# Kernel tuning notes

Measured on AMD Instinct MI355X. Metric: run time of the kernel, lower is better.

The kernel has to match this reference:

```python
import jax, jax.numpy as jnp
import numpy as np

B, S, E = 4, 2048, 1024
H, D = 16, 64
SCALE = D ** -0.5


def setup_inputs() -> dict:
    key = jax.random.key(0)
    ks = jax.random.split(key, 6)
    x = jax.random.normal(ks[0], (B, S, E), dtype=jnp.float32)
    # per-head projection weights stacked along head axis: [H, E, D]
    Wq = jax.random.normal(ks[1], (H, E, D), dtype=jnp.float32) * 0.02
    Wk = jax.random.normal(ks[2], (H, E, D), dtype=jnp.float32) * 0.02
    Wv = jax.random.normal(ks[3], (H, E, D), dtype=jnp.float32) * 0.02
    # output projection: concat(H*D) -> E, with bias (nn.Linear default)
    Wo = jax.random.normal(ks[4], (H * D, E), dtype=jnp.float32) * 0.02
    bo = jax.random.normal(ks[5], (E,), dtype=jnp.float32) * 0.02
    return {"x": x, "Wq": Wq, "Wk": Wk, "Wv": Wv, "Wo": Wo, "bo": bo}


def reference(x, Wq, Wk, Wv, Wo, bo):
    # batched QKV projections for all heads at once
    q = jnp.einsum('bse,hed->bhsd', x, Wq)
    k = jnp.einsum('bse,hed->bhsd', x, Wk)
    v = jnp.einsum('bse,hed->bhsd', x, Wv)
    # full (non-causal) attention, scores [b,h,s,s]
    scores = jnp.einsum('bhsd,bhtd->bhst', q, k) * SCALE
    attn = jax.nn.softmax(scores, axis=-1)
    o = jnp.einsum('bhst,bhtd->bhsd', attn, v)
    # concat heads in head order along feature dim -> [b,s,H*D]
    o = o.transpose(0, 2, 1, 3).reshape(x.shape[0], x.shape[1], -1)
    return o @ Wo + bo
```

## Files before the change

### kernel.cpp

```cpp
#include <hip/hip_runtime.h>
#include <hip/hip_fp16.h>
#include <stdint.h>

#define BB 4
#define SS 2048
#define EE 1024
#define HH 16
#define DD 64

typedef _Float16 half8 __attribute__((ext_vector_type(8)));
typedef __fp16 fp16x2 __attribute__((ext_vector_type(2)));
typedef float f32x2 __attribute__((ext_vector_type(2)));
typedef float f32x4 __attribute__((ext_vector_type(4)));
typedef float f32x16 __attribute__((ext_vector_type(16)));
typedef uint32_t u32;
typedef uint32_t u32x2 __attribute__((ext_vector_type(2)));

#define MFMA32(a, b, c) __builtin_amdgcn_mfma_f32_16x16x32_f16((a), (b), (c), 0, 0, 0)
#define MFMA3216(a, b, c) __builtin_amdgcn_mfma_f32_32x32x16_f16((a), (b), (c), 0, 0, 0)

#define GLD_LDS16(g, l)                                                        \
  __builtin_amdgcn_global_load_lds(                                            \
      (const __attribute__((address_space(1))) u32*)(const void*)(g),          \
      (__attribute__((address_space(3))) u32*)(void*)(l), 16, 0, 0)

static __device__ __forceinline__ u32 pkh(float a, float b) {
  union { fp16x2 h; u32 u; } z;
  z.h = __builtin_amdgcn_cvt_pkrtz(a, b);
  return z.u;
}

static __device__ __forceinline__ void plswap(u32& a, u32& b) {
  asm("v_permlane32_swap_b32 %0, %1" : "+v"(a), "+v"(b));
}

__global__ __launch_bounds__(256) void conv_x_k(const float* __restrict__ x,
                                                _Float16* __restrict__ xh) {
  size_t i = ((size_t)blockIdx.x * 256 + threadIdx.x) * 8;
  f32x4 a = *(const f32x4*)(x + i);
  f32x4 b = *(const f32x4*)(x + i + 4);
  half8 o;
  o[0] = (_Float16)a[0]; o[1] = (_Float16)a[1];
  o[2] = (_Float16)a[2]; o[3] = (_Float16)a[3];
  o[4] = (_Float16)b[0]; o[5] = (_Float16)b[1];
  o[6] = (_Float16)b[2]; o[7] = (_Float16)b[3];
  *(half8*)(xh + i) = o;
}

__global__ __launch_bounds__(256) void conv_w_k(const float* __restrict__ Wq,
                                                const float* __restrict__ Wk,
                                                const float* __restrict__ Wv,
                                                _Float16* __restrict__ Wt) {
  __shared__ float T[64][65];
  int bid = blockIdx.x;
  int sel = bid >> 8, rem = bid & 255;
  int h = rem >> 4, e0 = (rem & 15) * 64;
  const float* W = (sel == 0 ? Wq : sel == 1 ? Wk : Wv) + (size_t)h * EE * DD;
  float scale = (sel == 0) ? 0.18033688011112042f : 1.0f;
  int tid = threadIdx.x;
  {
    int e = tid >> 2, d0 = (tid & 3) * 16;
#pragma unroll
    for (int i = 0; i < 4; ++i) {
      f32x4 v = *(const f32x4*)(W + (size_t)(e0 + e) * DD + d0 + i * 4);
      T[e][d0 + i * 4 + 0] = v[0];
      T[e][d0 + i * 4 + 1] = v[1];
      T[e][d0 + i * 4 + 2] = v[2];
      T[e][d0 + i * 4 + 3] = v[3];
    }
  }
  __syncthreads();
  {
    int d = tid >> 2, c0 = (tid & 3) * 16;
    half8 o0, o1;
#pragma unroll
    for (int i = 0; i < 8; ++i) o0[i] = (_Float16)(T[c0 + i][d] * scale);
#pragma unroll
    for (int i = 0; i < 8; ++i) o1[i] = (_Float16)(T[c0 + 8 + i][d] * scale);
    _Float16* dst = Wt + ((size_t)sel * 1024 + h * 64 + d) * EE + e0 + c0;
    *(half8*)dst = o0;
    *(half8*)(dst + 8) = o1;
  }
}

__global__ __launch_bounds__(256) void conv_wo_k(const float* __restrict__ Wo,
                                                 _Float16* __restrict__ Wot) {
  __shared__ float T[64][65];
  int bid = blockIdx.x;
  int k0 = (bid >> 4) * 64, n0 = (bid & 15) * 64;
  int tid = threadIdx.x;
  {
    int k = tid >> 2, c0 = (tid & 3) * 16;
#pragma unroll
    for (int i = 0; i < 4; ++i) {
      f32x4 v = *(const f32x4*)(Wo + (size_t)(k0 + k) * EE + n0 + c0 + i * 4);
      T[k][c0 + i * 4 + 0] = v[0];
      T[k][c0 + i * 4 + 1] = v[1];
      T[k][c0 + i * 4 + 2] = v[2];
      T[k][c0 + i * 4 + 3] = v[3];
    }
  }
  __syncthreads();
  {
    int n = tid >> 2, c0 = (tid & 3) * 16;
    half8 o0, o1;
#pragma unroll
    for (int i = 0; i < 8; ++i) o0[i] = (_Float16)T[c0 + i][n];
#pragma unroll
    for (int i = 0; i < 8; ++i) o1[i] = (_Float16)T[c0 + 8 + i][n];
    _Float16* dst = Wot + (size_t)(n0 + n) * EE + k0 + c0;
    *(half8*)dst = o0;
    *(half8*)(dst + 8) = o1;
  }
}

__global__ __launch_bounds__(256, 3) void qkv_proj_k(
    const _Float16* __restrict__ xh, const _Float16* __restrict__ Wt,
    _Float16* __restrict__ qkv) {
  __shared__ __align__(16) _Float16 As[2][128 * 32];
  __shared__ __align__(16) _Float16 Bs[2][128 * 32];
  __shared__ __align__(16) _Float16 Tt[64][136];
  int bid0 = blockIdx.x;
  int bid = (bid0 & 7) * 192 + (bid0 >> 3);
  int nblk = bid % 24, mblk = bid / 24;
  int row0 = mblk * 128, n0 = nblk * 128;
  int tid = threadIdx.x, lane = tid & 63, w = tid >> 6;
  int wm = w >> 1, wn = w & 1;
  int l15 = lane & 15, lhi = lane >> 4;

  f32x4 acc[4][4];
#pragma unroll
  for (int i = 0; i < 4; ++i)
#pragma unroll
    for (int j = 0; j < 4; ++j) acc[i][j] = (f32x4){0.f, 0.f, 0.f, 0.f};

  const char* Ab = (const char*)xh + (size_t)row0 * 2048;
  const char* Bb = (const char*)Wt + (size_t)n0 * 2048;
  int ob0 = w * 1024 + lane * 16;

#define STAGE_AB(K0, BUF)                                                      \
  {                                                                            \
    GLD_LDS16(Ab + (size_t)(ob0 >> 6) * 2048 + (K0) * 2 + (ob0 & 63),          \
              (char*)As[BUF] + w * 1024);                                      \
    GLD_LDS16(Ab + (size_t)((ob0 + 4096) >> 6) * 2048 + (K0) * 2 + (ob0 & 63), \
              (char*)As[BUF] + 4096 + w * 1024);                               \
    GLD_LDS16(Bb + (size_t)(ob0 >> 6) * 2048 + (K0) * 2 + (ob0 & 63),          \
              (char*)Bs[BUF] + w * 1024);                                      \
    GLD_LDS16(Bb + (size_t)((ob0 + 4096) >> 6) * 2048 + (K0) * 2 + (ob0 & 63), \
              (char*)Bs[BUF] + 4096 + w * 1024);                               \
  }

  STAGE_AB(0, 0);
  __syncthreads();

  for (int k0 = 0; k0 < EE; k0 += 32) {
    int cur = (k0 >> 5) & 1;
    if (k0 + 32 < EE) STAGE_AB(k0 + 32, cur ^ 1);
    half8 a[4], b[4];
#pragma unroll
    for (int mf = 0; mf < 4; ++mf)
      a[mf] = *(const half8*)(As[cur] + (wm * 64 + mf * 16 + l15) * 32 + 8 * lhi);
#pragma unroll
    for (int nf = 0; nf < 4; ++nf)
      b[nf] = *(const half8*)(Bs[cur] + (wn * 64 + nf * 16 + l15) * 32 + 8 * lhi);
#pragma unroll
    for (int mf = 0; mf < 4; ++mf)
#pragma unroll
      for (int nf = 0; nf < 4; ++nf)
        acc[mf][nf] = MFMA32(a[mf], b[nf], acc[mf][nf]);
    __syncthreads();
  }
#undef STAGE_AB

  const size_t KOFF = (size_t)BB * HH * SS * DD;
  if (nblk < 16) {
#pragma unroll
    for (int mf = 0; mf < 4; ++mf)
#pragma unroll
      for (int nf = 0; nf < 4; ++nf)
#pragma unroll
        for (int r = 0; r < 4; ++r) {
          int row = row0 + wm * 64 + mf * 16 + 4 * lhi + r;
          int n = n0 + wn * 64 + nf * 16 + l15;
          int sel = n >> 10, hh = (n >> 6) & 15, d = n & 63;
          int b_ = row >> 11, s = row & 2047;
          qkv[(size_t)sel * KOFF + (((size_t)b_ * HH + hh) * SS + s) * DD + d] =
              (_Float16)acc[mf][nf][r];
        }
  } else {
    int b_ = row0 >> 11, sbase = row0 & 2047;
    _Float16* vout = qkv + 2 * KOFF;
#pragma unroll
    for (int half = 0; half < 2; ++half) {
      if (half) __syncthreads();
      if (wn == half) {
#pragma unroll
        for (int mf = 0; mf < 4; ++mf)
#pragma unroll
          for (int nf = 0; nf < 4; ++nf) {
            union { _Float16 h[4]; u32x2 v; } t4;
#pragma unroll
            for (int r = 0; r < 4; ++r) t4.h[r] = (_Float16)acc[mf][nf][r];
            *(u32x2*)&Tt[nf * 16 + l15][wm * 64 + mf * 16 + 4 * lhi] = t4.v;
          }
      }
      __syncthreads();
      int d = tid >> 2, c0 = (tid & 3) * 32;
      int head = ((n0 >> 6) + half) & 15;
      _Float16* dst =
          vout + ((size_t)((b_ * 16 + head) * 64 + d)) * SS + sbase + c0;
#pragma unroll
      for (int j = 0; j < 4; ++j)
        *(half8*)(dst + 8 * j) = *(const half8*)&Tt[d][c0 + 8 * j];
    }
  }
}

__global__ __launch_bounds__(256, 2) void attn_k(
    const _Float16* __restrict__ qkv, _Float16* __restrict__ ob) {
  __shared__ __align__(16) _Float16 Ks[2][64 * 64];
  __shared__ __align__(16) _Float16 Vs[2][64 * 64];

  const int bid0 = blockIdx.x;
  const int bid = (bid0 & 7) * 64 + (bid0 >> 3);
  const int bh = bid >> 3, qb = bid & 7;
  const int b_ = bh >> 4, h = bh & 15;
  const size_t KOFF = (size_t)BB * HH * SS * DD;
  const _Float16* qp = qkv + (size_t)bh * SS * DD;
  const char* kp = (const char*)(qkv + KOFF + (size_t)bh * SS * DD);
  const char* vtp = (const char*)(qkv + 2 * KOFF + (size_t)bh * DD * SS);

  const int tid = threadIdx.x, lane = tid & 63, w = tid >> 6;
  const int l31 = lane & 31, u = lane >> 5;
  const int q0 = qb * 256 + w * 64;

  half8 qf[4][2];
#pragma unroll
  for (int ekf = 0; ekf < 4; ++ekf)
#pragma unroll
    for (int nq = 0; nq < 2; ++nq)
      qf[ekf][nq] = *(const half8*)(qp +
          (size_t)(q0 + nq * 32 + l31) * DD + ekf * 16 + u * 8);

  f32x16 oa00 = {}, oa10 = {}, oa01 = {}, oa11 = {};
  f32x2 rs2_0 = {0.f, 0.f}, rs2_1 = {0.f, 0.f};

  const int trow = tid >> 3;
  const int scol = ((tid & 7) * 16) ^ (16 * (trow & 7));
  const int lds0 = tid * 16;
  const int xsw = 16 * (l31 & 7);
  const int NT = SS / 64;

#define STAGE_KV(IT, BUF)                                                      \
  {                                                                            \
    const char* sk_ = kp + (size_t)(IT) * 8192;                                \
    const char* sv_ = vtp + (size_t)(IT) * 128;                                \
    GLD_LDS16(sk_ + trow * 128 + scol, (char*)Ks[BUF] + lds0);                 \
    GLD_LDS16(sk_ + (trow + 32) * 128 + scol, (char*)Ks[BUF] + 4096 + lds0);   \
    GLD_LDS16(sv_ + (size_t)trow * 4096 + scol, (char*)Vs[BUF] + lds0);        \
    GLD_LDS16(sv_ + (size_t)(trow + 32) * 4096 + scol,                         \
              (char*)Vs[BUF] + 4096 + lds0);                                   \
  }

  STAGE_KV(0, 0);
  __syncthreads();

  for (int it = 0; it < NT; ++it) {
    const int cur = it & 1;
    if (it + 1 < NT) STAGE_KV(it + 1, cur ^ 1);
    const char* kb = (const char*)Ks[cur];
    const char* vb = (const char*)Vs[cur];

#pragma unroll
    for (int nt = 0; nt < 2; ++nt) {
      const char* krow = kb + (size_t)(32 * nt + l31) * 128;
      half8 kA0 = *(const half8*)(krow + ((16 * u) ^ xsw));
      half8 kA1 = *(const half8*)(krow + ((32 + 16 * u) ^ xsw));
      half8 kA2 = *(const half8*)(krow + ((64 + 16 * u) ^ xsw));
      half8 kA3 = *(const half8*)(krow + ((96 + 16 * u) ^ xsw));
      f32x16 s0 = {}, s1 = {};
      s0 = MFMA3216(kA0, qf[0][0], s0);
      s1 = MFMA3216(kA0, qf[0][1], s1);
      s0 = MFMA3216(kA1, qf[1][0], s0);
      s1 = MFMA3216(kA1, qf[1][1], s1);
      s0 = MFMA3216(kA2, qf[2][0], s0);
      s1 = MFMA3216(kA2, qf[2][1], s1);
      s0 = MFMA3216(kA3, qf[3][0], s0);
      s1 = MFMA3216(kA3, qf[3][1], s1);

      u32 w0[8], w1[8];
#pragma unroll
      for (int m = 0; m < 8; ++m) {
        float a0 = __builtin_amdgcn_exp2f(s0[2 * m]);
        float a1 = __builtin_amdgcn_exp2f(s0[2 * m + 1]);
        w0[m] = pkh(a0, a1);
        rs2_0 += (f32x2){a0, a1};
        float c0 = __builtin_amdgcn_exp2f(s1[2 * m]);
        float c1 = __builtin_amdgcn_exp2f(s1[2 * m + 1]);
        w1[m] = pkh(c0, c1);
        rs2_1 += (f32x2){c0, c1};
      }

#pragma unroll
      for (int kfl = 0; kfl < 2; ++kfl) {
        u32 p00 = w0[4 * kfl + 0], p02 = w0[4 * kfl + 2];
        u32 p01 = w0[4 * kfl + 1], p03 = w0[4 * kfl + 3];
        plswap(p00, p02);
        plswap(p01, p03);
        u32 p10 = w1[4 * kfl + 0], p12 = w1[4 * kfl + 2];
        u32 p11 = w1[4 * kfl + 1], p13 = w1[4 * kfl + 3];
        plswap(p10, p12);
        plswap(p11, p13);
        union { u32 q[4]; half8 h; } pb0, pb1;
        pb0.q[0] = p00; pb0.q[1] = p01; pb0.q[2] = p02; pb0.q[3] = p03;
        pb1.q[0] = p10; pb1.q[1] = p11; pb1.q[2] = p12; pb1.q[3] = p13;
        const int kf = 2 * nt + kfl;
        const char* vcol = vb + ((32 * kf + 16 * u) ^ xsw);
        half8 vA0 = *(const half8*)(vcol + (size_t)l31 * 128);
        half8 vA1 = *(const half8*)(vcol + (size_t)(32 + l31) * 128);
        oa00 = MFMA3216(vA0, pb0.h, oa00);
        oa10 = MFMA3216(vA1, pb0.h, oa10);
        oa01 = MFMA3216(vA0, pb1.h, oa01);
        oa11 = MFMA3216(vA1, pb1.h, oa11);
      }
    }
    __syncthreads();
  }
#undef STAGE_KV

  float rs0 = rs2_0.x + rs2_0.y;
  float rs1 = rs2_1.x + rs2_1.y;
  float inv0 = 1.0f / (rs0 + __shfl_xor(rs0, 32, 64));
  float inv1 = 1.0f / (rs1 + __shfl_xor(rs1, 32, 64));

#define STORE_OA(OA, MD, NQ, INV)                                              \
  {                                                                            \
    _Float16* dst = ob + (size_t)(b_ * SS + q0 + 32 * (NQ) + l31) * 1024 +     \
                    h * 64 + 32 * (MD) + 4 * u;                                \
    _Pragma("unroll")                                                          \
    for (int rr = 0; rr < 4; ++rr) {                                           \
      u32x2 pr;                                                                \
      pr.x = pkh(OA[4 * rr + 0] * (INV), OA[4 * rr + 1] * (INV));              \
      pr.y = pkh(OA[4 * rr + 2] * (INV), OA[4 * rr + 3] * (INV));              \
      *(u32x2*)(dst + 8 * rr) = pr;                                            \
    }                                                                          \
  }
  STORE_OA(oa00, 0, 0, inv0)
  STORE_OA(oa10, 1, 0, inv0)
  STORE_OA(oa01, 0, 1, inv1)
  STORE_OA(oa11, 1, 1, inv1)
#undef STORE_OA
}

__global__ __launch_bounds__(256, 3) void oproj_k(
    const _Float16* __restrict__ ob, const _Float16* __restrict__ Wot,
    const float* __restrict__ bo, float* __restrict__ out) {
  __shared__ __align__(16) _Float16 As[2][128 * 32];
  __shared__ __align__(16) _Float16 Bs[2][128 * 32];
  int bid0 = blockIdx.x;
  int bid = (bid0 & 7) * 64 + (bid0 >> 3);
  int nblk = bid & 7, mblk = bid >> 3;
  int row0 = mblk * 128, n0 = nblk * 128;
  int tid = threadIdx.x, lane = tid & 63, w = tid >> 6;
  int wm = w >> 1, wn = w & 1;
  int l15 = lane & 15, lhi = lane >> 4;

  f32x4 acc[4][4];
#pragma unroll
  for (int i = 0; i < 4; ++i)
#pragma unroll
    for (int j = 0; j < 4; ++j) acc[i][j] = (f32x4){0.f, 0.f, 0.f, 0.f};

  const char* Ab = (const char*)ob + (size_t)row0 * 2048;
  const char* Bb = (const char*)Wot + (size_t)n0 * 2048;
  int ob0 = w * 1024 + lane * 16;

#define STAGE_AB(K0, BUF)                                                      \
  {                                                                            \
    GLD_LDS16(Ab + (size_t)(ob0 >> 6) * 2048 + (K0) * 2 + (ob0 & 63),          \
              (char*)As[BUF] + w * 1024);                                      \
    GLD_LDS16(Ab + (size_t)((ob0 + 4096) >> 6) * 2048 + (K0) * 2 + (ob0 & 63), \
              (char*)As[BUF] + 4096 + w * 1024);                               \
    GLD_LDS16(Bb + (size_t)(ob0 >> 6) * 2048 + (K0) * 2 + (ob0 & 63),          \
              (char*)Bs[BUF] + w * 1024);                                      \
    GLD_LDS16(Bb + (size_t)((ob0 + 4096) >> 6) * 2048 + (K0) * 2 + (ob0 & 63), \
              (char*)Bs[BUF] + 4096 + w * 1024);                               \
  }

  STAGE_AB(0, 0);
  __syncthreads();

  for (int k0 = 0; k0 < EE; k0 += 32) {
    int cur = (k0 >> 5) & 1;
    if (k0 + 32 < EE) STAGE_AB(k0 + 32, cur ^ 1);
    half8 a[4], b[4];
#pragma unroll
    for (int mf = 0; mf < 4; ++mf)
      a[mf] = *(const half8*)(As[cur] + (wm * 64 + mf * 16 + l15) * 32 + 8 * lhi);
#pragma unroll
    for (int nf = 0; nf < 4; ++nf)
      b[nf] = *(const half8*)(Bs[cur] + (wn * 64 + nf * 16 + l15) * 32 + 8 * lhi);
#pragma unroll
    for (int mf = 0; mf < 4; ++mf)
#pragma unroll
      for (int nf = 0; nf < 4; ++nf)
        acc[mf][nf] = MFMA32(a[mf], b[nf], acc[mf][nf]);
    __syncthreads();
  }
#undef STAGE_AB

#pragma unroll
  for (int mf = 0; mf < 4; ++mf)
#pragma unroll
    for (int nf = 0; nf < 4; ++nf) {
      int n = n0 + wn * 64 + nf * 16 + l15;
      float bias = bo[n];
#pragma unroll
      for (int r = 0; r < 4; ++r) {
        int row = row0 + wm * 64 + mf * 16 + 4 * lhi + r;
        out[(size_t)row * EE + n] = acc[mf][nf][r] + bias;
      }
    }
}

extern "C" void kernel_launch(void* const* d_in, const int* in_sizes, int n_in,
                              void* d_out, int out_size, void* d_ws, size_t ws_size,
                              hipStream_t stream) {
  const float* x  = (const float*)d_in[0];
  const float* Wq = (const float*)d_in[1];
  const float* Wk = (const float*)d_in[2];
  const float* Wv = (const float*)d_in[3];
  const float* Wo = (const float*)d_in[4];
  const float* bo = (const float*)d_in[5];
  float* out = (float*)d_out;

  const size_t KOFF = (size_t)BB * HH * SS * DD;
  _Float16* qkv = (_Float16*)d_ws;
  _Float16* obuf = qkv + 3 * KOFF;
  _Float16* xh = (_Float16*)d_out;
  _Float16* Wt = xh + (size_t)BB * SS * EE;
  _Float16* Wot = qkv;

  conv_x_k<<<dim3(4096), dim3(256), 0, stream>>>(x, xh);
  conv_w_k<<<dim3(768), dim3(256), 0, stream>>>(Wq, Wk, Wv, Wt);
  qkv_proj_k<<<dim3(64 * 24), dim3(256), 0, stream>>>(xh, Wt, qkv);
  attn_k<<<dim3(512), dim3(256), 0, stream>>>(qkv, obuf);
  conv_wo_k<<<dim3(256), dim3(256), 0, stream>>>(Wo, Wot);
  oproj_k<<<dim3(64 * 8), dim3(256), 0, stream>>>(obuf, Wot, bo, out);
}
```

Before: 187.3 us.

## Split attention KV range across two blocks and merge partials in combine kernel

Each attention block now handles half the key/value sequence, doubling the grid to 1024 blocks with a higher launch-bounds occupancy target. Each half writes normalized partial outputs and its row sums to scratch space. A new combine kernel merges the halves with weights derived from those sums before the output projection. The goal is more resident waves per CU to hide latency. The cost is an extra kernel with a full read/write pass over the attention output, and possible register pressure or spills under the tighter occupancy bound.

```diff
diff --git a/kernel.cpp b/kernel.cpp
--- a/kernel.cpp
+++ b/kernel.cpp
@@ -216,14 +216,15 @@
   }
 }
 
-__global__ __launch_bounds__(256, 2) void attn_k(
-    const _Float16* __restrict__ qkv, _Float16* __restrict__ ob) {
+__global__ __launch_bounds__(256, 4) void attn_k(
+    const _Float16* __restrict__ qkv, _Float16* __restrict__ op0,
+    _Float16* __restrict__ op1, float* __restrict__ rsb) {
   __shared__ __align__(16) _Float16 Ks[2][64 * 64];
   __shared__ __align__(16) _Float16 Vs[2][64 * 64];
 
   const int bid0 = blockIdx.x;
-  const int bid = (bid0 & 7) * 64 + (bid0 >> 3);
-  const int bh = bid >> 3, qb = bid & 7;
+  const int bid = (bid0 & 7) * 128 + (bid0 >> 3);
+  const int bh = bid >> 4, qb = (bid >> 1) & 7, th = bid & 1;
   const int b_ = bh >> 4, h = bh & 15;
   const size_t KOFF = (size_t)BB * HH * SS * DD;
   const _Float16* qp = qkv + (size_t)bh * SS * DD;
@@ -249,12 +250,13 @@
   const int scol = ((tid & 7) * 16) ^ (16 * (trow & 7));
   const int lds0 = tid * 16;
   const int xsw = 16 * (l31 & 7);
-  const int NT = SS / 64;
-
-#define STAGE_KV(IT, BUF)                                                      \
+  const int NTH = SS / 128;
+  const int T0 = th * NTH;
+
+#define STAGE_KV(T, BUF)                                                       \
   {                                                                            \
-    const char* sk_ = kp + (size_t)(IT) * 8192;                                \
-    const char* sv_ = vtp + (size_t)(IT) * 128;                                \
+    const char* sk_ = kp + (size_t)(T) * 8192;                                 \
+    const char* sv_ = vtp + (size_t)(T) * 128;                                 \
     GLD_LDS16(sk_ + trow * 128 + scol, (char*)Ks[BUF] + lds0);                 \
     GLD_LDS16(sk_ + (trow + 32) * 128 + scol, (char*)Ks[BUF] + 4096 + lds0);   \
     GLD_LDS16(sv_ + (size_t)trow * 4096 + scol, (char*)Vs[BUF] + lds0);        \
@@ -262,12 +264,12 @@
               (char*)Vs[BUF] + 4096 + lds0);                                   \
   }
 
-  STAGE_KV(0, 0);
+  STAGE_KV(T0, 0);
   __syncthreads();
 
-  for (int it = 0; it < NT; ++it) {
+  for (int it = 0; it < NTH; ++it) {
     const int cur = it & 1;
-    if (it + 1 < NT) STAGE_KV(it + 1, cur ^ 1);
+    if (it + 1 < NTH) STAGE_KV(T0 + it + 1, cur ^ 1);
     const char* kb = (const char*)Ks[cur];
     const char* vb = (const char*)Vs[cur];
 
@@ -330,12 +332,21 @@
 
   float rs0 = rs2_0.x + rs2_0.y;
   float rs1 = rs2_1.x + rs2_1.y;
-  float inv0 = 1.0f / (rs0 + __shfl_xor(rs0, 32, 64));
-  float inv1 = 1.0f / (rs1 + __shfl_xor(rs1, 32, 64));
+  float tot0 = rs0 + __shfl_xor(rs0, 32, 64);
+  float tot1 = rs1 + __shfl_xor(rs1, 32, 64);
+  float inv0 = 1.0f / tot0;
+  float inv1 = 1.0f / tot1;
+
+  _Float16* op = th ? op1 : op0;
+  float* rsp = rsb + (size_t)th * 64 * SS + (size_t)bh * SS;
+  if (u == 0) {
+    rsp[q0 + l31] = tot0;
+    rsp[q0 + 32 + l31] = tot1;
+  }
 
 #define STORE_OA(OA, MD, NQ, INV)                                              \
   {                                                                            \
-    _Float16* dst = ob + (size_t)(b_ * SS + q0 + 32 * (NQ) + l31) * 1024 +     \
+    _Float16* dst = op + (size_t)(b_ * SS + q0 + 32 * (NQ) + l31) * 1024 +     \
                     h * 64 + 32 * (MD) + 4 * u;                                \
     _Pragma("unroll")                                                          \
     for (int rr = 0; rr < 4; ++rr) {                                           \
@@ -350,6 +361,26 @@
   STORE_OA(oa01, 0, 1, inv1)
   STORE_OA(oa11, 1, 1, inv1)
 #undef STORE_OA
+}
+
+__global__ __launch_bounds__(256) void combine_k(
+    const _Float16* __restrict__ op0, const _Float16* __restrict__ op1,
+    const float* __restrict__ rs, _Float16* __restrict__ ob) {
+  size_t i = ((size_t)blockIdx.x * 256 + threadIdx.x) * 8;
+  int b = (int)(i >> 21);
+  int s = (int)(i >> 10) & 2047;
+  int h = (int)(i >> 6) & 15;
+  int bhq = (((b << 4) | h) << 11) | s;
+  float r0 = rs[bhq], r1 = rs[(64 << 11) + bhq];
+  float wn = 1.0f / (r0 + r1);
+  float w0 = r0 * wn, w1 = r1 * wn;
+  half8 a = *(const half8*)(op0 + i);
+  half8 c = *(const half8*)(op1 + i);
+  half8 o;
+#pragma unroll
+  for (int j = 0; j < 8; ++j)
+    o[j] = (_Float16)((float)a[j] * w0 + (float)c[j] * w1);
+  *(half8*)(ob + i) = o;
 }
 
 __global__ __launch_bounds__(256, 3) void oproj_k(
@@ -435,16 +466,20 @@
   float* out = (float*)d_out;
 
   const size_t KOFF = (size_t)BB * HH * SS * DD;
+  const size_t OBN = (size_t)BB * SS * EE;
   _Float16* qkv = (_Float16*)d_ws;
   _Float16* obuf = qkv + 3 * KOFF;
   _Float16* xh = (_Float16*)d_out;
-  _Float16* Wt = xh + (size_t)BB * SS * EE;
+  _Float16* Wt = xh + OBN;
+  _Float16* op1 = (_Float16*)d_out;
+  float* rsb = (float*)((char*)d_out + OBN * 2);
   _Float16* Wot = qkv;
 
   conv_x_k<<<dim3(4096), dim3(256), 0, stream>>>(x, xh);
   conv_w_k<<<dim3(768), dim3(256), 0, stream>>>(Wq, Wk, Wv, Wt);
   qkv_proj_k<<<dim3(64 * 24), dim3(256), 0, stream>>>(xh, Wt, qkv);
-  attn_k<<<dim3(512), dim3(256), 0, stream>>>(qkv, obuf);
+  attn_k<<<dim3(1024), dim3(256), 0, stream>>>(qkv, obuf, op1, rsb);
+  combine_k<<<dim3(4096), dim3(256), 0, stream>>>(obuf, op1, rsb, obuf);
   conv_wo_k<<<dim3(256), dim3(256), 0, stream>>>(Wo, Wot);
   oproj_k<<<dim3(64 * 8), dim3(256), 0, stream>>>(obuf, Wot, bo, out);
 }
```

New measurement: 325.1 us. 1.74x slower.

## Halve per-wave query rows in attention to double grid and occupancy

Applied to the files above, without the earlier changes.

The attention kernel now gives each wave 32 query rows instead of 64, so each block covers 128 queries and the grid grows from 512 to 1024 blocks, with launch bounds raised to 4 blocks per CU. This lowers register pressure (fewer accumulators and score tiles) so more waves can hide latency, and 1024 blocks fill the 256 CUs better. In exchange, each K/V tile loaded into LDS is reused by half as many queries, which doubles total K/V traffic and the K/V LDS reads per query.

```diff
diff --git a/kernel.cpp b/kernel.cpp
--- a/kernel.cpp
+++ b/kernel.cpp
@@ -216,14 +216,14 @@
   }
 }
 
-__global__ __launch_bounds__(256, 2) void attn_k(
+__global__ __launch_bounds__(256, 4) void attn_k(
     const _Float16* __restrict__ qkv, _Float16* __restrict__ ob) {
   __shared__ __align__(16) _Float16 Ks[2][64 * 64];
   __shared__ __align__(16) _Float16 Vs[2][64 * 64];
 
   const int bid0 = blockIdx.x;
-  const int bid = (bid0 & 7) * 64 + (bid0 >> 3);
-  const int bh = bid >> 3, qb = bid & 7;
+  const int bid = (bid0 & 7) * 128 + (bid0 >> 3);
+  const int bh = bid >> 4, qb = bid & 15;
   const int b_ = bh >> 4, h = bh & 15;
   const size_t KOFF = (size_t)BB * HH * SS * DD;
   const _Float16* qp = qkv + (size_t)bh * SS * DD;
@@ -232,18 +232,15 @@
 
   const int tid = threadIdx.x, lane = tid & 63, w = tid >> 6;
   const int l31 = lane & 31, u = lane >> 5;
-  const int q0 = qb * 256 + w * 64;
-
-  half8 qf[4][2];
+  const int q0 = qb * 128 + w * 32;
+
+  half8 qf[4];
 #pragma unroll
   for (int ekf = 0; ekf < 4; ++ekf)
-#pragma unroll
-    for (int nq = 0; nq < 2; ++nq)
-      qf[ekf][nq] = *(const half8*)(qp +
-          (size_t)(q0 + nq * 32 + l31) * DD + ekf * 16 + u * 8);
-
-  f32x16 oa00 = {}, oa10 = {}, oa01 = {}, oa11 = {};
-  f32x2 rs2_0 = {0.f, 0.f}, rs2_1 = {0.f, 0.f};
+    qf[ekf] = *(const half8*)(qp + (size_t)(q0 + l31) * DD + ekf * 16 + u * 8);
+
+  f32x16 oa0 = {}, oa1 = {};
+  f32x2 rs2 = {0.f, 0.f};
 
   const int trow = tid >> 3;
   const int scol = ((tid & 7) * 16) ^ (16 * (trow & 7));
@@ -278,27 +275,19 @@
       half8 kA1 = *(const half8*)(krow + ((32 + 16 * u) ^ xsw));
       half8 kA2 = *(const half8*)(krow + ((64 + 16 * u) ^ xsw));
       half8 kA3 = *(const half8*)(krow + ((96 + 16 * u) ^ xsw));
-      f32x16 s0 = {}, s1 = {};
-      s0 = MFMA3216(kA0, qf[0][0], s0);
-      s1 = MFMA3216(kA0, qf[0][1], s1);
-      s0 = MFMA3216(kA1, qf[1][0], s0);
-      s1 = MFMA3216(kA1, qf[1][1], s1);
-      s0 = MFMA3216(kA2, qf[2][0], s0);
-      s1 = MFMA3216(kA2, qf[2][1], s1);
-      s0 = MFMA3216(kA3, qf[3][0], s0);
-      s1 = MFMA3216(kA3, qf[3][1], s1);
-
-      u32 w0[8], w1[8];
+      f32x16 s0 = {};
+      s0 = MFMA3216(kA0, qf[0], s0);
+      s0 = MFMA3216(kA1, qf[1], s0);
+      s0 = MFMA3216(kA2, qf[2], s0);
+      s0 = MFMA3216(kA3, qf[3], s0);
+
+      u32 w0[8];
 #pragma unroll
       for (int m = 0; m < 8; ++m) {
         float a0 = __builtin_amdgcn_exp2f(s0[2 * m]);
         float a1 = __builtin_amdgcn_exp2f(s0[2 * m + 1]);
         w0[m] = pkh(a0, a1);
-        rs2_0 += (f32x2){a0, a1};
-        float c0 = __builtin_amdgcn_exp2f(s1[2 * m]);
-        float c1 = __builtin_amdgcn_exp2f(s1[2 * m + 1]);
-        w1[m] = pkh(c0, c1);
-        rs2_1 += (f32x2){c0, c1};
+        rs2 += (f32x2){a0, a1};
       }
 
 #pragma unroll
@@ -307,48 +296,37 @@
         u32 p01 = w0[4 * kfl + 1], p03 = w0[4 * kfl + 3];
         plswap(p00, p02);
         plswap(p01, p03);
-        u32 p10 = w1[4 * kfl + 0], p12 = w1[4 * kfl + 2];
-        u32 p11 = w1[4 * kfl + 1], p13 = w1[4 * kfl + 3];
-        plswap(p10, p12);
-        plswap(p11, p13);
-        union { u32 q[4]; half8 h; } pb0, pb1;
-        pb0.q[0] = p00; pb0.q[1] = p01; pb0.q[2] = p02; pb0.q[3] = p03;
-        pb1.q[0] = p10; pb1.q[1] = p11; pb1.q[2] = p12; pb1.q[3] = p13;
+        union { u32 q[4]; half8 h; } pb;
+        pb.q[0] = p00; pb.q[1] = p01; pb.q[2] = p02; pb.q[3] = p03;
         const int kf = 2 * nt + kfl;
         const char* vcol = vb + ((32 * kf + 16 * u) ^ xsw);
         half8 vA0 = *(const half8*)(vcol + (size_t)l31 * 128);
         half8 vA1 = *(const half8*)(vcol + (size_t)(32 + l31) * 128);
-        oa00 = MFMA3216(vA0, pb0.h, oa00);
-        oa10 = MFMA3216(vA1, pb0.h, oa10);
-        oa01 = MFMA3216(vA0, pb1.h, oa01);
-        oa11 = MFMA3216(vA1, pb1.h, oa11);
+        oa0 = MFMA3216(vA0, pb.h, oa0);
+        oa1 = MFMA3216(vA1, pb.h, oa1);
       }
     }
     __syncthreads();
   }
 #undef STAGE_KV
 
-  float rs0 = rs2_0.x + rs2_0.y;
-  float rs1 = rs2_1.x + rs2_1.y;
-  float inv0 = 1.0f / (rs0 + __shfl_xor(rs0, 32, 64));
-  float inv1 = 1.0f / (rs1 + __shfl_xor(rs1, 32, 64));
-
-#define STORE_OA(OA, MD, NQ, INV)                                              \
+  float rs0 = rs2.x + rs2.y;
+  float inv = 1.0f / (rs0 + __shfl_xor(rs0, 32, 64));
+
+#define STORE_OA(OA, MD)                                                       \
   {                                                                            \
-    _Float16* dst = ob + (size_t)(b_ * SS + q0 + 32 * (NQ) + l31) * 1024 +     \
+    _Float16* dst = ob + (size_t)(b_ * SS + q0 + l31) * 1024 +                 \
                     h * 64 + 32 * (MD) + 4 * u;                                \
     _Pragma("unroll")                                                          \
     for (int rr = 0; rr < 4; ++rr) {                                           \
       u32x2 pr;                                                                \
-      pr.x = pkh(OA[4 * rr + 0] * (INV), OA[4 * rr + 1] * (INV));              \
-      pr.y = pkh(OA[4 * rr + 2] * (INV), OA[4 * rr + 3] * (INV));              \
+      pr.x = pkh(OA[4 * rr + 0] * inv, OA[4 * rr + 1] * inv);                  \
+      pr.y = pkh(OA[4 * rr + 2] * inv, OA[4 * rr + 3] * inv);                  \
       *(u32x2*)(dst + 8 * rr) = pr;                                            \
     }                                                                          \
   }
-  STORE_OA(oa00, 0, 0, inv0)
-  STORE_OA(oa10, 1, 0, inv0)
-  STORE_OA(oa01, 0, 1, inv1)
-  STORE_OA(oa11, 1, 1, inv1)
+  STORE_OA(oa0, 0)
+  STORE_OA(oa1, 1)
 #undef STORE_OA
 }
 
@@ -444,7 +422,7 @@
   conv_x_k<<<dim3(4096), dim3(256), 0, stream>>>(x, xh);
   conv_w_k<<<dim3(768), dim3(256), 0, stream>>>(Wq, Wk, Wv, Wt);
   qkv_proj_k<<<dim3(64 * 24), dim3(256), 0, stream>>>(xh, Wt, qkv);
-  attn_k<<<dim3(512), dim3(256), 0, stream>>>(qkv, obuf);
+  attn_k<<<dim3(1024), dim3(256), 0, stream>>>(qkv, obuf);
   conv_wo_k<<<dim3(256), dim3(256), 0, stream>>>(Wo, Wot);
   oproj_k<<<dim3(64 * 8), dim3(256), 0, stream>>>(obuf, Wot, bo, out);
 }
```

New measurement: 193.3 us. 3.2% more time.
